# Kernel optimization log

Measured on AMD Instinct MI355X. Metric: run time of the kernel, lower is better.

Reference implementation:

```python
import jax, jax.numpy as jnp
import numpy as np

TOPK = 30  # from init_kwargs


def setup_inputs() -> dict:
    key = jax.random.key(0)
    k1, k2, k3 = jax.random.split(key, 3)
    BH, N, D = 32, 2048, 64  # (batch*heads, seq_len, head_dim)
    return {
        "q": jax.random.normal(k1, (BH, N, D), dtype=jnp.float32),
        "k": jax.random.normal(k2, (BH, N, D), dtype=jnp.float32),
        "v": jax.random.normal(k3, (BH, N, D), dtype=jnp.float32),
        "B": 2048,          # == seq_len N (used for mask shape in original)
        "num_heads": 8,     # unused by the math, kept for signature parity
    }


def reference(q, k, v, B, num_heads):
    # scores: [BH, N, N]  (torch.bmm(q, k.transpose(1,2)))
    scores = jnp.einsum('bnd,bmd->bnm', q, k)
    # scale=None and attn_mask=None in the default call -> both branches skipped
    BH, N, _ = scores.shape
    # top-k per row, scatter 1.0 into a zero mask (faithful to torch.scatter_)
    _, idx = jax.lax.top_k(scores, TOPK)                      # [BH, N, TOPK]
    bi = jnp.arange(BH)[:, None, None]
    ri = jnp.arange(N)[None, :, None]
    keep = jnp.zeros((BH, N, N), dtype=bool).at[bi, ri, idx].set(True)
    # masked softmax over last axis (dim=2)
    masked = jnp.where(keep, scores, -jnp.inf)
    attn = jax.nn.softmax(masked, axis=-1)
    # dropout p=0.0 -> identity
    context = jnp.einsum('bnm,bmd->bnd', attn, v)
    return context, attn
```

## Files before the change

kernel.cpp:

```cpp
#include <hip/hip_runtime.h>
#include <hip/hip_bf16.h>

#define BHn 32
#define Nn 2048
#define Dn 64
#define KSEL 30
#define CAP 112
#define RB 128
#define CT 64
#define ZTH 1.80f

typedef short bf16x8 __attribute__((ext_vector_type(8)));
typedef float f32x4 __attribute__((ext_vector_type(4)));
typedef unsigned long long u64;

__device__ __forceinline__ unsigned ford(float x) {
  unsigned b = __float_as_uint(x);
  return (b & 0x80000000u) ? ~b : (b | 0x80000000u);
}
__device__ __forceinline__ float unford(unsigned u) {
  unsigned b = (u & 0x80000000u) ? (u & 0x7fffffffu) : ~u;
  return __uint_as_float(b);
}
__device__ __forceinline__ u64 umax64(u64 a, u64 b) { return a > b ? a : b; }

__device__ __forceinline__ void split2(float a, float b, ushort2& hi, ushort2& lo) {
  __hip_bfloat162 h = __float22bfloat162_rn(make_float2(a, b));
  union { __hip_bfloat162 v; ushort2 u; } ch; ch.v = h;
  hi = ch.u;
  float2 hf = __bfloat1622float2(h);
  __hip_bfloat162 l = __float22bfloat162_rn(make_float2(a - hf.x, b - hf.y));
  union { __hip_bfloat162 v; ushort2 u; } cl; cl.v = l;
  lo = cl.u;
}

__global__ __launch_bounds__(256, 3) void score_cand(
    const float* __restrict__ q, const float* __restrict__ k,
    u64* __restrict__ cand, unsigned* __restrict__ counts) {
  __shared__ ushort qh[RB][64], ql[RB][64];
  __shared__ ushort kh[CT][64], kl[CT][64];
  __shared__ unsigned ccnt[RB];
  __shared__ float tf[RB];

  const int t = threadIdx.x;
  const int bid = blockIdx.x;
  const int bh = (bid & 7) * 4 + ((bid >> 3) & 3);
  const int rb = bid >> 5;
  const int lane = t & 63, w = t >> 6;
  const int m16 = lane & 15, quad = lane >> 4;

  const float* qb = q + ((size_t)bh * Nn + rb * RB) * Dn;
  const float* kb = k + (size_t)bh * Nn * Dn;
  const size_t growbase = (size_t)bh * Nn + (size_t)rb * RB;

#pragma unroll
  for (int i = 0; i < 8; ++i) {
    int c = t + 256 * i;
    int row = c >> 4, f4 = c & 15;
    float4 a = *(const float4*)(qb + row * Dn + f4 * 4);
    int sp = (((f4 >> 1) ^ (row & 7)) << 1) | (f4 & 1);
    ushort2 h0, l0, h1, l1;
    split2(a.x, a.y, h0, l0);
    split2(a.z, a.w, h1, l1);
    *(ushort4*)&qh[row][sp * 4] = make_ushort4(h0.x, h0.y, h1.x, h1.y);
    *(ushort4*)&ql[row][sp * 4] = make_ushort4(l0.x, l0.y, l1.x, l1.y);
  }
  if (t < RB) {
    const float* qr = qb + t * Dn;
    float ss = 0.f;
#pragma unroll
    for (int i = 0; i < 16; ++i) {
      float4 a = *(const float4*)(qr + i * 4);
      ss = fmaf(a.x, a.x, ss); ss = fmaf(a.y, a.y, ss);
      ss = fmaf(a.z, a.z, ss); ss = fmaf(a.w, a.w, ss);
    }
    tf[t] = ZTH * sqrtf(ss);
    ccnt[t] = 0u;
  }
  __syncthreads();

  unsigned tfr[2][4];
#pragma unroll
  for (int mt = 0; mt < 2; ++mt)
#pragma unroll
    for (int rg = 0; rg < 4; ++rg)
      tfr[mt][rg] = ford(tf[w * 32 + mt * 16 + quad * 4 + rg]);

  for (int ct = 0; ct < Nn / CT; ++ct) {
    __syncthreads();
#pragma unroll
    for (int i = 0; i < 4; ++i) {
      int c = t + 256 * i;
      int row = c >> 4, f4 = c & 15;
      float4 a = *(const float4*)(kb + (size_t)(ct * CT + row) * Dn + f4 * 4);
      int sp = (((f4 >> 1) ^ (row & 7)) << 1) | (f4 & 1);
      ushort2 h0, l0, h1, l1;
      split2(a.x, a.y, h0, l0);
      split2(a.z, a.w, h1, l1);
      *(ushort4*)&kh[row][sp * 4] = make_ushort4(h0.x, h0.y, h1.x, h1.y);
      *(ushort4*)&kl[row][sp * 4] = make_ushort4(l0.x, l0.y, l1.x, l1.y);
    }
    __syncthreads();

    f32x4 acc[2][4];
#pragma unroll
    for (int mt = 0; mt < 2; ++mt)
#pragma unroll
      for (int nt = 0; nt < 4; ++nt) acc[mt][nt] = (f32x4){0.f, 0.f, 0.f, 0.f};

#pragma unroll
    for (int ks = 0; ks < 2; ++ks) {
      bf16x8 aH[2], aL[2], bH[4], bL[4];
#pragma unroll
      for (int mt = 0; mt < 2; ++mt) {
        int r = w * 32 + mt * 16 + m16;
        int ch = (ks * 4 + quad) ^ (r & 7);
        aH[mt] = *(const bf16x8*)&qh[r][ch * 8];
        aL[mt] = *(const bf16x8*)&ql[r][ch * 8];
      }
#pragma unroll
      for (int nt = 0; nt < 4; ++nt) {
        int rr = nt * 16 + m16;
        int ch = (ks * 4 + quad) ^ (rr & 7);
        bH[nt] = *(const bf16x8*)&kh[rr][ch * 8];
        bL[nt] = *(const bf16x8*)&kl[rr][ch * 8];
      }
#pragma unroll
      for (int mt = 0; mt < 2; ++mt)
#pragma unroll
        for (int nt = 0; nt < 4; ++nt) {
          acc[mt][nt] = __builtin_amdgcn_mfma_f32_16x16x32_bf16(aL[mt], bH[nt], acc[mt][nt], 0, 0, 0);
          acc[mt][nt] = __builtin_amdgcn_mfma_f32_16x16x32_bf16(aH[mt], bL[nt], acc[mt][nt], 0, 0, 0);
          acc[mt][nt] = __builtin_amdgcn_mfma_f32_16x16x32_bf16(aH[mt], bH[nt], acc[mt][nt], 0, 0, 0);
        }
    }

#pragma unroll
    for (int mt = 0; mt < 2; ++mt)
#pragma unroll
      for (int rg = 0; rg < 4; ++rg) {
        unsigned tk = tfr[mt][rg];
        int rl = w * 32 + mt * 16 + quad * 4 + rg;
#pragma unroll
        for (int nt = 0; nt < 4; ++nt) {
          float s = acc[mt][nt][rg];
          unsigned fk = ford(s);
          if (fk > tk) {
            unsigned pos = atomicAdd(&ccnt[rl], 1u);
            if (pos < CAP) {
              int col = ct * CT + nt * 16 + m16;
              cand[(growbase + rl) * CAP + pos] =
                  ((u64)fk << 32) | (unsigned)(2047 - col);
            }
          }
        }
      }
  }
  __syncthreads();
  if (t < RB) counts[growbase + t] = ccnt[t];
}

__global__ __launch_bounds__(256) void select_rows(
    u64* __restrict__ cand, const unsigned* __restrict__ counts,
    const float* __restrict__ v, float* __restrict__ ctx,
    unsigned* __restrict__ flags) {
  __shared__ u64 scr[4][CAP];
  const int lane = threadIdx.x & 63, wv = threadIdx.x >> 6;
  const size_t gr = (size_t)blockIdx.x * 4 + wv;
  const int bh = (int)(gr >> 11);

  const int C = (int)counts[gr];
  const bool bad = (C < KSEL) || (C > CAP);
  if (lane == 0) flags[gr] = bad ? 1u : 0u;
  if (bad) return;

  u64* sw_ = scr[wv];
  for (int p = lane; p < C; p += 64) sw_[p] = cand[gr * CAP + p];

  const int slots = (C + 63) >> 6;
  u64 mykey[2] = {0ull, 0ull};
  int rk[2] = {CAP, CAP};
  float es[2] = {0.f, 0.f};
  u64 mymax = 0ull;
#pragma unroll
  for (int tt = 0; tt < 2; ++tt) {
    if (tt < slots) {
      int p = lane + 64 * tt;
      mykey[tt] = (p < C) ? sw_[p] : 0ull;
      mymax = umax64(mymax, mykey[tt]);
    }
  }
#pragma unroll
  for (int off = 32; off; off >>= 1) mymax = umax64(mymax, __shfl_xor(mymax, off));
  const float mrow = unford((unsigned)(mymax >> 32));

#pragma unroll 1
  for (int tt = 0; tt < slots; ++tt) {
    int r = 0;
    u64 me = mykey[tt];
    for (int jj = 0; jj < C; ++jj) r += (sw_[jj] > me);
    rk[tt] = r;
  }
  float z = 0.f;
#pragma unroll
  for (int tt = 0; tt < 2; ++tt) {
    int p = lane + 64 * tt;
    bool sel = (tt < slots) && (p < C) && (rk[tt] < KSEL);
    es[tt] = sel ? __expf(unford((unsigned)(mykey[tt] >> 32)) - mrow) : 0.f;
    z += es[tt];
  }
#pragma unroll
  for (int off = 32; off; off >>= 1) z += __shfl_xor(z, off);
  const float invZ = 1.f / z;

#pragma unroll
  for (int tt = 0; tt < 2; ++tt) {
    int p = lane + 64 * tt;
    if (tt < slots && p < C && rk[tt] < KSEL) {
      float wt = es[tt] * invZ;
      unsigned col = 2047u - (unsigned)(mykey[tt] & 0xffffffffu);
      u64 e = ((u64)__float_as_uint(wt) << 32) | col;
      sw_[rk[tt]] = e;
      cand[gr * CAP + rk[tt]] = e;
    }
  }
  const float* vb = v + (size_t)bh * Nn * Dn;
  float a = 0.f;
#pragma unroll
  for (int p = 0; p < KSEL; ++p) {
    u64 e = sw_[p];
    a = fmaf(__uint_as_float((unsigned)(e >> 32)), vb[(e & 0x7ffull) * Dn + lane], a);
  }
  ctx[gr * Dn + lane] = a;
}

__global__ __launch_bounds__(256) void repair_rows(
    const float* __restrict__ q, const float* __restrict__ k,
    const float* __restrict__ v, float* __restrict__ ctx,
    u64* __restrict__ cand, const unsigned* __restrict__ flags) {
  __shared__ float sc2[Nn];
  __shared__ u64 red[256];
  __shared__ float qrow[Dn];
  __shared__ int selc[KSEL];
  __shared__ float selv[KSEL];
  __shared__ float zsh;
  __shared__ unsigned flagbuf[256];

  const int t = threadIdx.x;
  const int base = blockIdx.x * 256;
  flagbuf[t] = flags[base + t];
  __syncthreads();

  for (int i = 0; i < 256; ++i) {
    if (flagbuf[i] == 0u) continue;
    const int gr = base + i;
    const int bh = gr >> 11;
    if (t < Dn) qrow[t] = q[(size_t)gr * Dn + t];
    __syncthreads();
    const float* kb = k + (size_t)bh * Nn * Dn;
#pragma unroll
    for (int j = 0; j < 8; ++j) {
      int col = t + 256 * j;
      float s = 0.f;
      for (int d = 0; d < Dn; d += 4) {
        float4 kk = *(const float4*)(kb + (size_t)col * Dn + d);
        s = fmaf(qrow[d], kk.x, s);
        s = fmaf(qrow[d + 1], kk.y, s);
        s = fmaf(qrow[d + 2], kk.z, s);
        s = fmaf(qrow[d + 3], kk.w, s);
      }
      sc2[col] = s;
    }
    __syncthreads();
    for (int p = 0; p < KSEL; ++p) {
      u64 best = 0ull;
#pragma unroll
      for (int j = 0; j < 8; ++j) {
        int col = t + 256 * j;
        u64 kk = ((u64)ford(sc2[col]) << 32) | (unsigned)(2047 - col);
        best = umax64(best, kk);
      }
      red[t] = best;
      __syncthreads();
      for (int off = 128; off; off >>= 1) {
        if (t < off) red[t] = umax64(red[t], red[t + off]);
        __syncthreads();
      }
      if (t == 0) {
        u64 b = red[0];
        int col = 2047 - (int)(b & 0xffffffffu);
        selc[p] = col;
        selv[p] = unford((unsigned)(b >> 32));
        sc2[col] = -3.4e38f;
      }
      __syncthreads();
    }
    if (t == 0) {
      float m = selv[0], zz = 0.f;
      for (int p = 0; p < KSEL; ++p) zz += __expf(selv[p] - m);
      zsh = 1.f / zz;
    }
    __syncthreads();
    if (t < KSEL) {
      float wt = __expf(selv[t] - selv[0]) * zsh;
      cand[(size_t)gr * CAP + t] = ((u64)__float_as_uint(wt) << 32) | (unsigned)selc[t];
    }
    if (t < Dn) {
      const float* vb = v + (size_t)bh * Nn * Dn;
      float a = 0.f;
      for (int p = 0; p < KSEL; ++p)
        a = fmaf(__expf(selv[p] - selv[0]) * zsh, vb[(size_t)selc[p] * Dn + t], a);
      ctx[(size_t)gr * Dn + t] = a;
    }
    __syncthreads();
  }
}

__global__ __launch_bounds__(256) void fill_attn(
    const u64* __restrict__ cand, float* __restrict__ attn) {
  __shared__ float lrow[4 * Nn];
  const int t = threadIdx.x;
  const size_t row0 = (size_t)blockIdx.x * 4;

#pragma unroll
  for (int i = 0; i < 8; ++i)
    *(float4*)&lrow[i * 1024 + t * 4] = make_float4(0.f, 0.f, 0.f, 0.f);
  __syncthreads();
  if (t < 4 * KSEL) {
    int r = t / KSEL, p = t - r * KSEL;
    u64 e = cand[(row0 + r) * CAP + p];
    lrow[r * Nn + (int)(e & 0x7ffull)] = __uint_as_float((unsigned)(e >> 32));
  }
  __syncthreads();
  float* ab = attn + row0 * Nn;
#pragma unroll
  for (int i = 0; i < 8; ++i)
    *(float4*)(ab + i * 1024 + t * 4) = *(const float4*)&lrow[i * 1024 + t * 4];
}

extern "C" void kernel_launch(void* const* d_in, const int* in_sizes, int n_in,
                              void* d_out, int out_size, void* d_ws,
                              size_t ws_size, hipStream_t stream) {
  const float* q = (const float*)d_in[0];
  const float* k = (const float*)d_in[1];
  const float* v = (const float*)d_in[2];
  float* out = (float*)d_out;
  float* ctx = out;
  float* attn = out + (size_t)BHn * Nn * Dn;

  unsigned* counts = (unsigned*)d_ws;
  unsigned* flags = counts + (size_t)BHn * Nn;
  u64* cand = (u64*)((char*)d_ws + (size_t)BHn * Nn * 8);

  score_cand<<<dim3(BHn * Nn / RB), 256, 0, stream>>>(q, k, cand, counts);
  select_rows<<<dim3(BHn * Nn / 4), 256, 0, stream>>>(cand, counts, v, ctx, flags);
  repair_rows<<<dim3(BHn * Nn / 256), 256, 0, stream>>>(q, k, v, ctx, cand, flags);
  fill_attn<<<dim3(BHn * Nn / 4), 256, 0, stream>>>(cand, attn);
}
```

Measured before the change: 860.8 us.

## Fuse attention fill into row selection and register-prefetch K tiles

Merges the fill_attn kernel into select_rows. Each block builds its four dense attention rows in shared memory and writes them with nontemporal stores, which removes one launch and the extra pass over the candidate buffer. The repair kernel now scatters its weights straight into attn after the dense rows are written. score_cand also prefetches the next K tile into registers during the MFMA work, which adds register pressure and moves the barrier to the end of the loop.

```diff
diff --git a/kernel.cpp b/kernel.cpp
--- a/kernel.cpp
+++ b/kernel.cpp
@@ -77,9 +77,16 @@
     tf[t] = ZTH * sqrtf(ss);
     ccnt[t] = 0u;
   }
+
+  unsigned tfr[2][4];
+  float4 pre[4];
+#pragma unroll
+  for (int i = 0; i < 4; ++i) {
+    int c = t + 256 * i;
+    pre[i] = *(const float4*)(kb + (size_t)(c >> 4) * Dn + (c & 15) * 4);
+  }
   __syncthreads();
 
-  unsigned tfr[2][4];
 #pragma unroll
   for (int mt = 0; mt < 2; ++mt)
 #pragma unroll
@@ -87,12 +94,11 @@
       tfr[mt][rg] = ford(tf[w * 32 + mt * 16 + quad * 4 + rg]);
 
   for (int ct = 0; ct < Nn / CT; ++ct) {
-    __syncthreads();
 #pragma unroll
     for (int i = 0; i < 4; ++i) {
       int c = t + 256 * i;
       int row = c >> 4, f4 = c & 15;
-      float4 a = *(const float4*)(kb + (size_t)(ct * CT + row) * Dn + f4 * 4);
+      float4 a = pre[i];
       int sp = (((f4 >> 1) ^ (row & 7)) << 1) | (f4 & 1);
       ushort2 h0, l0, h1, l1;
       split2(a.x, a.y, h0, l0);
@@ -101,6 +107,14 @@
       *(ushort4*)&kl[row][sp * 4] = make_ushort4(l0.x, l0.y, l1.x, l1.y);
     }
     __syncthreads();
+
+    if (ct + 1 < Nn / CT) {
+#pragma unroll
+      for (int i = 0; i < 4; ++i) {
+        int c = t + 256 * i;
+        pre[i] = *(const float4*)(kb + (size_t)((ct + 1) * CT + (c >> 4)) * Dn + (c & 15) * 4);
+      }
+    }
 
     f32x4 acc[2][4];
 #pragma unroll
@@ -155,89 +169,105 @@
           }
         }
       }
-  }
-  __syncthreads();
+    __syncthreads();
+  }
   if (t < RB) counts[growbase + t] = ccnt[t];
 }
 
-__global__ __launch_bounds__(256) void select_rows(
+__global__ __launch_bounds__(256) void select_fill(
     u64* __restrict__ cand, const unsigned* __restrict__ counts,
     const float* __restrict__ v, float* __restrict__ ctx,
-    unsigned* __restrict__ flags) {
+    float* __restrict__ attn, unsigned* __restrict__ flags) {
+  __shared__ float lrow[4 * Nn];
   __shared__ u64 scr[4][CAP];
-  const int lane = threadIdx.x & 63, wv = threadIdx.x >> 6;
-  const size_t gr = (size_t)blockIdx.x * 4 + wv;
+  const int t = threadIdx.x;
+  const int lane = t & 63, wv = t >> 6;
+  const size_t row0 = (size_t)blockIdx.x * 4;
+  const size_t gr = row0 + wv;
   const int bh = (int)(gr >> 11);
+
+#pragma unroll
+  for (int i = 0; i < 8; ++i)
+    *(f32x4*)&lrow[i * 1024 + t * 4] = (f32x4){0.f, 0.f, 0.f, 0.f};
 
   const int C = (int)counts[gr];
   const bool bad = (C < KSEL) || (C > CAP);
   if (lane == 0) flags[gr] = bad ? 1u : 0u;
-  if (bad) return;
-
-  u64* sw_ = scr[wv];
-  for (int p = lane; p < C; p += 64) sw_[p] = cand[gr * CAP + p];
-
-  const int slots = (C + 63) >> 6;
-  u64 mykey[2] = {0ull, 0ull};
-  int rk[2] = {CAP, CAP};
-  float es[2] = {0.f, 0.f};
-  u64 mymax = 0ull;
-#pragma unroll
-  for (int tt = 0; tt < 2; ++tt) {
-    if (tt < slots) {
+
+  if (!bad) {
+    u64* sw_ = scr[wv];
+    for (int p = lane; p < C; p += 64) sw_[p] = cand[gr * CAP + p];
+
+    const int slots = (C + 63) >> 6;
+    u64 mykey[2] = {0ull, 0ull};
+    int rk[2] = {CAP, CAP};
+    float es[2] = {0.f, 0.f};
+    u64 mymax = 0ull;
+#pragma unroll
+    for (int tt = 0; tt < 2; ++tt) {
+      if (tt < slots) {
+        int p = lane + 64 * tt;
+        mykey[tt] = (p < C) ? sw_[p] : 0ull;
+        mymax = umax64(mymax, mykey[tt]);
+      }
+    }
+#pragma unroll
+    for (int off = 32; off; off >>= 1) mymax = umax64(mymax, __shfl_xor(mymax, off));
+    const float mrow = unford((unsigned)(mymax >> 32));
+
+#pragma unroll 1
+    for (int tt = 0; tt < slots; ++tt) {
+      int r = 0;
+      u64 me = mykey[tt];
+      for (int jj = 0; jj < C; ++jj) r += (sw_[jj] > me);
+      rk[tt] = r;
+    }
+    float z = 0.f;
+#pragma unroll
+    for (int tt = 0; tt < 2; ++tt) {
       int p = lane + 64 * tt;
-      mykey[tt] = (p < C) ? sw_[p] : 0ull;
-      mymax = umax64(mymax, mykey[tt]);
-    }
-  }
-#pragma unroll
-  for (int off = 32; off; off >>= 1) mymax = umax64(mymax, __shfl_xor(mymax, off));
-  const float mrow = unford((unsigned)(mymax >> 32));
-
-#pragma unroll 1
-  for (int tt = 0; tt < slots; ++tt) {
-    int r = 0;
-    u64 me = mykey[tt];
-    for (int jj = 0; jj < C; ++jj) r += (sw_[jj] > me);
-    rk[tt] = r;
-  }
-  float z = 0.f;
-#pragma unroll
-  for (int tt = 0; tt < 2; ++tt) {
-    int p = lane + 64 * tt;
-    bool sel = (tt < slots) && (p < C) && (rk[tt] < KSEL);
-    es[tt] = sel ? __expf(unford((unsigned)(mykey[tt] >> 32)) - mrow) : 0.f;
-    z += es[tt];
-  }
-#pragma unroll
-  for (int off = 32; off; off >>= 1) z += __shfl_xor(z, off);
-  const float invZ = 1.f / z;
-
-#pragma unroll
-  for (int tt = 0; tt < 2; ++tt) {
-    int p = lane + 64 * tt;
-    if (tt < slots && p < C && rk[tt] < KSEL) {
-      float wt = es[tt] * invZ;
-      unsigned col = 2047u - (unsigned)(mykey[tt] & 0xffffffffu);
-      u64 e = ((u64)__float_as_uint(wt) << 32) | col;
-      sw_[rk[tt]] = e;
-      cand[gr * CAP + rk[tt]] = e;
-    }
-  }
-  const float* vb = v + (size_t)bh * Nn * Dn;
-  float a = 0.f;
-#pragma unroll
-  for (int p = 0; p < KSEL; ++p) {
-    u64 e = sw_[p];
-    a = fmaf(__uint_as_float((unsigned)(e >> 32)), vb[(e & 0x7ffull) * Dn + lane], a);
-  }
-  ctx[gr * Dn + lane] = a;
+      bool sel = (tt < slots) && (p < C) && (rk[tt] < KSEL);
+      es[tt] = sel ? __expf(unford((unsigned)(mykey[tt] >> 32)) - mrow) : 0.f;
+      z += es[tt];
+    }
+#pragma unroll
+    for (int off = 32; off; off >>= 1) z += __shfl_xor(z, off);
+    const float invZ = 1.f / z;
+
+#pragma unroll
+    for (int tt = 0; tt < 2; ++tt) {
+      int p = lane + 64 * tt;
+      if (tt < slots && p < C && rk[tt] < KSEL) {
+        float wt = es[tt] * invZ;
+        int col = 2047 - (int)(mykey[tt] & 0xffffffffu);
+        u64 e = ((u64)__float_as_uint(wt) << 32) | (unsigned)col;
+        sw_[rk[tt]] = e;
+        lrow[wv * Nn + col] = wt;
+      }
+    }
+    const float* vb = v + (size_t)bh * Nn * Dn;
+    float a = 0.f;
+#pragma unroll
+    for (int p = 0; p < KSEL; ++p) {
+      u64 e = sw_[p];
+      a = fmaf(__uint_as_float((unsigned)(e >> 32)), vb[(e & 0x7ffull) * Dn + lane], a);
+    }
+    ctx[gr * Dn + lane] = a;
+  }
+  __syncthreads();
+
+  float* ab = attn + row0 * Nn;
+#pragma unroll
+  for (int i = 0; i < 8; ++i) {
+    f32x4 vv = *(const f32x4*)&lrow[i * 1024 + t * 4];
+    __builtin_nontemporal_store(vv, (f32x4*)(ab + i * 1024 + t * 4));
+  }
 }
 
 __global__ __launch_bounds__(256) void repair_rows(
     const float* __restrict__ q, const float* __restrict__ k,
     const float* __restrict__ v, float* __restrict__ ctx,
-    u64* __restrict__ cand, const unsigned* __restrict__ flags) {
+    float* __restrict__ attn, const unsigned* __restrict__ flags) {
   __shared__ float sc2[Nn];
   __shared__ u64 red[256];
   __shared__ float qrow[Dn];
@@ -301,10 +331,8 @@
       zsh = 1.f / zz;
     }
     __syncthreads();
-    if (t < KSEL) {
-      float wt = __expf(selv[t] - selv[0]) * zsh;
-      cand[(size_t)gr * CAP + t] = ((u64)__float_as_uint(wt) << 32) | (unsigned)selc[t];
-    }
+    if (t < KSEL)
+      attn[(size_t)gr * Nn + selc[t]] = __expf(selv[t] - selv[0]) * zsh;
     if (t < Dn) {
       const float* vb = v + (size_t)bh * Nn * Dn;
       float a = 0.f;
@@ -314,28 +342,6 @@
     }
     __syncthreads();
   }
-}
-
-__global__ __launch_bounds__(256) void fill_attn(
-    const u64* __restrict__ cand, float* __restrict__ attn) {
-  __shared__ float lrow[4 * Nn];
-  const int t = threadIdx.x;
-  const size_t row0 = (size_t)blockIdx.x * 4;
-
-#pragma unroll
-  for (int i = 0; i < 8; ++i)
-    *(float4*)&lrow[i * 1024 + t * 4] = make_float4(0.f, 0.f, 0.f, 0.f);
-  __syncthreads();
-  if (t < 4 * KSEL) {
-    int r = t / KSEL, p = t - r * KSEL;
-    u64 e = cand[(row0 + r) * CAP + p];
-    lrow[r * Nn + (int)(e & 0x7ffull)] = __uint_as_float((unsigned)(e >> 32));
-  }
-  __syncthreads();
-  float* ab = attn + row0 * Nn;
-#pragma unroll
-  for (int i = 0; i < 8; ++i)
-    *(float4*)(ab + i * 1024 + t * 4) = *(const float4*)&lrow[i * 1024 + t * 4];
 }
 
 extern "C" void kernel_launch(void* const* d_in, const int* in_sizes, int n_in,
@@ -353,7 +359,6 @@
   u64* cand = (u64*)((char*)d_ws + (size_t)BHn * Nn * 8);
 
   score_cand<<<dim3(BHn * Nn / RB), 256, 0, stream>>>(q, k, cand, counts);
-  select_rows<<<dim3(BHn * Nn / 4), 256, 0, stream>>>(cand, counts, v, ctx, flags);
-  repair_rows<<<dim3(BHn * Nn / 256), 256, 0, stream>>>(q, k, v, ctx, cand, flags);
-  fill_attn<<<dim3(BHn * Nn / 4), 256, 0, stream>>>(cand, attn);
-}
+  select_fill<<<dim3(BHn * Nn / 4), 256, 0, stream>>>(cand, counts, v, ctx, attn, flags);
+  repair_rows<<<dim3(BHn * Nn / 256), 256, 0, stream>>>(q, k, v, ctx, attn, flags);
+}
```

New measurement: 804.0 us. -6.6%, faster.
